# Performance work log

Hardware: AMD Instinct MI355X
Metric: run time of the kernel (lower is better)

The kernel has to match this reference:

```python
import jax, jax.numpy as jnp
import numpy as np

B, NQ, H = 65536, 32, 1024  # batch, n_qubits, hidden_dim


def setup_inputs() -> dict:
    key = jax.random.key(0)
    k1, k2, k3 = jax.random.split(key, 3)
    x = jax.random.normal(k1, (B, NQ), dtype=jnp.float32)  # rotation angles per qubit
    # nn.Linear(n_qubits, hidden_dim) parameters
    W = jax.random.normal(k2, (H, NQ), dtype=jnp.float32) / np.sqrt(NQ).astype(np.float32)
    b = jax.random.normal(k3, (H,), dtype=jnp.float32) * 0.01
    return {"x": x, "W": W, "b": b}


def reference(x, W, b):
    # Exact analytic simulation of the Pennylane circuit.
    # Starting from |0...0>, RY(theta_i) puts qubit i in cos(theta_i/2)|0> + sin(theta_i/2)|1>.
    # In the Heisenberg picture, the CNOT chain CNOT(0,1)...CNOT(n-2,n-1) maps
    #   Z_k -> Z_0 Z_1 ... Z_k,
    # and on the RY product state <Z_j> = cos(theta_j), so
    #   <Z_k> = prod_{j<=k} cos(theta_j)  (exact, identical math to the statevector sim).
    z = jnp.cumprod(jnp.cos(x), axis=-1)  # [B, n_qubits] expectation values
    # per-sample linear layer, batched as one GEMM (original loops over batch in Python)
    return z @ W.T + b  # [B, hidden_dim]
```

## Files before the change

kernel.cpp:

```cpp
#include <hip/hip_runtime.h>
#include <hip/hip_bf16.h>


#define B_TOT 65536
#define NQ    32
#define H_TOT 1024
#define BM    32
#define BN    128

typedef float v4f __attribute__((ext_vector_type(4)));

__global__ __launch_bounds__(256) void qlayer_kernel(
    const float* __restrict__ x,
    const float* __restrict__ W,
    const float* __restrict__ bias,
    float* __restrict__ out)
{
    __shared__ float zs[BM * NQ];
    __shared__ float wlds[NQ * BN];

    const int tid = threadIdx.x;
    const int b0  = blockIdx.x * BM;
    const int h0  = blockIdx.y * BN;

    const float4* wg = reinterpret_cast<const float4*>(W + h0 * NQ);
    float4 wv[4];
#pragma unroll
    for (int i = 0; i < 4; ++i) wv[i] = wg[i * 256 + tid];

    const int g = tid >> 5;
    const int l = tid & 31;
#pragma unroll
    for (int p = 0; p < 4; ++p) {
        const int row = p * 8 + g;
        float v = __cosf(x[(b0 + row) * NQ + l]);
#pragma unroll
        for (int d = 1; d < 32; d <<= 1) {
            float o = __shfl_up(v, d, 32);
            if (l >= d) v *= o;
        }
        zs[row * NQ + l] = v;
    }

#pragma unroll
    for (int i = 0; i < 4; ++i) {
        const int idx = i * 256 + tid;
        const int h   = idx >> 3;
        const int k0  = (idx & 7) << 2;
        wlds[(k0 + 0) * BN + h] = wv[i].x;
        wlds[(k0 + 1) * BN + h] = wv[i].y;
        wlds[(k0 + 2) * BN + h] = wv[i].z;
        wlds[(k0 + 3) * BN + h] = wv[i].w;
    }
    __syncthreads();

    const int rg = tid >> 5;
    const int c4 = (tid & 31) << 2;

    float acc[4][4];
#pragma unroll
    for (int r = 0; r < 4; ++r)
#pragma unroll
        for (int c = 0; c < 4; ++c) acc[r][c] = 0.f;

#pragma unroll
    for (int k0 = 0; k0 < NQ; k0 += 4) {
        const float4 w0 = *reinterpret_cast<const float4*>(&wlds[(k0 + 0) * BN + c4]);
        const float4 w1 = *reinterpret_cast<const float4*>(&wlds[(k0 + 1) * BN + c4]);
        const float4 w2 = *reinterpret_cast<const float4*>(&wlds[(k0 + 2) * BN + c4]);
        const float4 w3 = *reinterpret_cast<const float4*>(&wlds[(k0 + 3) * BN + c4]);
#pragma unroll
        for (int r = 0; r < 4; ++r) {
            const float4 z4 = *reinterpret_cast<const float4*>(&zs[(rg * 4 + r) * NQ + k0]);
            acc[r][0] += z4.x * w0.x + z4.y * w1.x + z4.z * w2.x + z4.w * w3.x;
            acc[r][1] += z4.x * w0.y + z4.y * w1.y + z4.z * w2.y + z4.w * w3.y;
            acc[r][2] += z4.x * w0.z + z4.y * w1.z + z4.z * w2.z + z4.w * w3.z;
            acc[r][3] += z4.x * w0.w + z4.y * w1.w + z4.z * w2.w + z4.w * w3.w;
        }
    }

    const float4 bv = *reinterpret_cast<const float4*>(&bias[h0 + c4]);
#pragma unroll
    for (int r = 0; r < 4; ++r) {
        v4f o;
        o.x = acc[r][0] + bv.x;
        o.y = acc[r][1] + bv.y;
        o.z = acc[r][2] + bv.z;
        o.w = acc[r][3] + bv.w;
        v4f* dst = reinterpret_cast<v4f*>(
            &out[(size_t)(b0 + rg * 4 + r) * H_TOT + h0 + c4]);
        __builtin_nontemporal_store(o, dst);
    }
}

extern "C" void kernel_launch(void* const* d_in, const int* in_sizes, int n_in,
                              void* d_out, int out_size, void* d_ws, size_t ws_size,
                              hipStream_t stream) {
    const float* x = (const float*)d_in[0];
    const float* W = (const float*)d_in[1];
    const float* b = (const float*)d_in[2];
    float* out = (float*)d_out;

    dim3 grid(B_TOT / BM, H_TOT / BN);
    dim3 block(256);
    qlayer_kernel<<<grid, block, 0, stream>>>(x, W, b, out);
}
```

Before: 335.5 us.

## Split cumprod scan into separate kernel and keep W rows in registers

The cosine cumulative product now runs in its own kernel that writes z to workspace. A second GEMM kernel holds two full W rows per thread in registers and loops over 64 rows, reading z with uniform broadcast loads and storing two output columns per thread. This removes the shared-memory staging and the block-wide barrier, and stops W from being reloaded for every 32-row tile. In exchange it adds a second launch and a round trip of z through global memory, and the output stores become narrower 8-byte writes.

```diff
diff --git a/kernel.cpp b/kernel.cpp
--- a/kernel.cpp
+++ b/kernel.cpp
@@ -5,91 +5,70 @@
 #define B_TOT 65536
 #define NQ    32
 #define H_TOT 1024
-#define BM    32
-#define BN    128
+#define ROWS_PER_BLK 64
+#define COLS_PER_BLK 512
 
-typedef float v4f __attribute__((ext_vector_type(4)));
+typedef float v2f __attribute__((ext_vector_type(2)));
 
-__global__ __launch_bounds__(256) void qlayer_kernel(
+__global__ __launch_bounds__(256) void zscan_kernel(
     const float* __restrict__ x,
+    float* __restrict__ z)
+{
+    const int g = threadIdx.x >> 5;
+    const int l = threadIdx.x & 31;
+    const int row = blockIdx.x * 8 + g;
+    float v = __cosf(x[row * NQ + l]);
+#pragma unroll
+    for (int d = 1; d < 32; d <<= 1) {
+        float o = __shfl_up(v, d, 32);
+        if (l >= d) v *= o;
+    }
+    z[row * NQ + l] = v;
+}
+
+__global__ __launch_bounds__(256) void gemm_kernel(
+    const float* __restrict__ z,
     const float* __restrict__ W,
     const float* __restrict__ bias,
     float* __restrict__ out)
 {
-    __shared__ float zs[BM * NQ];
-    __shared__ float wlds[NQ * BN];
+    const int tid = threadIdx.x;
+    const int r0  = blockIdx.x * ROWS_PER_BLK;
+    const int c0  = blockIdx.y * COLS_PER_BLK + tid * 2;
 
-    const int tid = threadIdx.x;
-    const int b0  = blockIdx.x * BM;
-    const int h0  = blockIdx.y * BN;
+    float w0[NQ], w1[NQ];
+    const float4* wg0 = reinterpret_cast<const float4*>(W + (size_t)c0 * NQ);
+    const float4* wg1 = reinterpret_cast<const float4*>(W + (size_t)(c0 + 1) * NQ);
+#pragma unroll
+    for (int i = 0; i < 8; ++i) {
+        float4 a = wg0[i];
+        w0[4*i+0] = a.x; w0[4*i+1] = a.y; w0[4*i+2] = a.z; w0[4*i+3] = a.w;
+        float4 b = wg1[i];
+        w1[4*i+0] = b.x; w1[4*i+1] = b.y; w1[4*i+2] = b.z; w1[4*i+3] = b.w;
+    }
+    const float b0 = bias[c0];
+    const float b1 = bias[c0 + 1];
 
-    const float4* wg = reinterpret_cast<const float4*>(W + h0 * NQ);
-    float4 wv[4];
+    const float4* zp = reinterpret_cast<const float4*>(z + (size_t)r0 * NQ);
+    float* op = out + (size_t)r0 * H_TOT + c0;
+
+#pragma unroll 1
+    for (int r = 0; r < ROWS_PER_BLK; ++r) {
+        float zk[NQ];
 #pragma unroll
-    for (int i = 0; i < 4; ++i) wv[i] = wg[i * 256 + tid];
-
-    const int g = tid >> 5;
-    const int l = tid & 31;
+        for (int i = 0; i < 8; ++i) {
+            float4 t = zp[r * 8 + i];
+            zk[4*i+0] = t.x; zk[4*i+1] = t.y; zk[4*i+2] = t.z; zk[4*i+3] = t.w;
+        }
+        float a0 = b0, a1 = b1;
 #pragma unroll
-    for (int p = 0; p < 4; ++p) {
-        const int row = p * 8 + g;
-        float v = __cosf(x[(b0 + row) * NQ + l]);
-#pragma unroll
-        for (int d = 1; d < 32; d <<= 1) {
-            float o = __shfl_up(v, d, 32);
-            if (l >= d) v *= o;
+        for (int k = 0; k < NQ; ++k) {
+            a0 += zk[k] * w0[k];
+            a1 += zk[k] * w1[k];
         }
-        zs[row * NQ + l] = v;
-    }
-
-#pragma unroll
-    for (int i = 0; i < 4; ++i) {
-        const int idx = i * 256 + tid;
-        const int h   = idx >> 3;
-        const int k0  = (idx & 7) << 2;
-        wlds[(k0 + 0) * BN + h] = wv[i].x;
-        wlds[(k0 + 1) * BN + h] = wv[i].y;
-        wlds[(k0 + 2) * BN + h] = wv[i].z;
-        wlds[(k0 + 3) * BN + h] = wv[i].w;
-    }
-    __syncthreads();
-
-    const int rg = tid >> 5;
-    const int c4 = (tid & 31) << 2;
-
-    float acc[4][4];
-#pragma unroll
-    for (int r = 0; r < 4; ++r)
-#pragma unroll
-        for (int c = 0; c < 4; ++c) acc[r][c] = 0.f;
-
-#pragma unroll
-    for (int k0 = 0; k0 < NQ; k0 += 4) {
-        const float4 w0 = *reinterpret_cast<const float4*>(&wlds[(k0 + 0) * BN + c4]);
-        const float4 w1 = *reinterpret_cast<const float4*>(&wlds[(k0 + 1) * BN + c4]);
-        const float4 w2 = *reinterpret_cast<const float4*>(&wlds[(k0 + 2) * BN + c4]);
-        const float4 w3 = *reinterpret_cast<const float4*>(&wlds[(k0 + 3) * BN + c4]);
-#pragma unroll
-        for (int r = 0; r < 4; ++r) {
-            const float4 z4 = *reinterpret_cast<const float4*>(&zs[(rg * 4 + r) * NQ + k0]);
-            acc[r][0] += z4.x * w0.x + z4.y * w1.x + z4.z * w2.x + z4.w * w3.x;
-            acc[r][1] += z4.x * w0.y + z4.y * w1.y + z4.z * w2.y + z4.w * w3.y;
-            acc[r][2] += z4.x * w0.z + z4.y * w1.z + z4.z * w2.z + z4.w * w3.z;
-            acc[r][3] += z4.x * w0.w + z4.y * w1.w + z4.z * w2.w + z4.w * w3.w;
-        }
-    }
-
-    const float4 bv = *reinterpret_cast<const float4*>(&bias[h0 + c4]);
-#pragma unroll
-    for (int r = 0; r < 4; ++r) {
-        v4f o;
-        o.x = acc[r][0] + bv.x;
-        o.y = acc[r][1] + bv.y;
-        o.z = acc[r][2] + bv.z;
-        o.w = acc[r][3] + bv.w;
-        v4f* dst = reinterpret_cast<v4f*>(
-            &out[(size_t)(b0 + rg * 4 + r) * H_TOT + h0 + c4]);
-        __builtin_nontemporal_store(o, dst);
+        v2f o; o.x = a0; o.y = a1;
+        __builtin_nontemporal_store(o,
+            reinterpret_cast<v2f*>(op + (size_t)r * H_TOT));
     }
 }
 
@@ -100,8 +79,9 @@
     const float* W = (const float*)d_in[1];
     const float* b = (const float*)d_in[2];
     float* out = (float*)d_out;
+    float* z   = (float*)d_ws;
 
-    dim3 grid(B_TOT / BM, H_TOT / BN);
-    dim3 block(256);
-    qlayer_kernel<<<grid, block, 0, stream>>>(x, W, b, out);
+    zscan_kernel<<<dim3(B_TOT / 8), dim3(256), 0, stream>>>(x, z);
+    gemm_kernel<<<dim3(B_TOT / ROWS_PER_BLK, H_TOT / COLS_PER_BLK),
+                  dim3(256), 0, stream>>>(z, W, b, out);
 }
```

After: 302.3 us. -9.9%, faster.
